# Kernel optimization log

Measured on AMD Instinct MI355X. Metric: run time of the kernel, lower is better.

Reference implementation:

```python
import jax, jax.numpy as jnp
import numpy as np

N, E = 100000, 1600000
F1, H1, H2 = 128, 128, 128


def setup_inputs() -> dict:
    key = jax.random.key(0)
    ks = jax.random.split(key, 8)
    x = jax.random.normal(ks[0], (N, F1), dtype=jnp.float32)
    edge_index = jax.random.randint(ks[1], (2, E), 0, N, dtype=jnp.int64)
    s1 = 1.0 / np.sqrt(F1)
    s2 = 1.0 / np.sqrt(H1)
    s3 = 1.0 / np.sqrt(H2)
    W1 = jax.random.uniform(ks[2], (F1, H1), jnp.float32, -s1, s1)
    b1 = jax.random.uniform(ks[3], (H1,), jnp.float32, -s1, s1)
    W2 = jax.random.uniform(ks[4], (H1, H2), jnp.float32, -s2, s2)
    b2 = jax.random.uniform(ks[5], (H2,), jnp.float32, -s2, s2)
    Wc = jax.random.uniform(ks[6], (H2, 1), jnp.float32, -s3, s3)
    bc = jax.random.uniform(ks[7], (1,), jnp.float32, -s3, s3)
    return {"x": x, "edge_index": edge_index, "W1": W1, "b1": b1,
            "W2": W2, "b2": b2, "Wc": Wc, "bc": bc}


def _gcn_conv(h, W, b, row, col, norm, n):
    # linear transform then degree-normalized gather/scatter-add aggregation
    h = h @ W                                  # [N, out]
    msg = h[row] * norm[:, None]               # [E+N, out] gather + scale
    out = jax.ops.segment_sum(msg, col, num_segments=n)  # scatter-add
    return out + b


def reference(x, edge_index, W1, b1, W2, b2, Wc, bc):
    n = x.shape[0]
    loops = jnp.arange(n, dtype=edge_index.dtype)
    row = jnp.concatenate([edge_index[0], loops])  # sources (with self-loops)
    col = jnp.concatenate([edge_index[1], loops])  # targets (with self-loops)
    deg = jax.ops.segment_sum(jnp.ones_like(col, dtype=x.dtype), col,
                              num_segments=n)
    dinv = jnp.where(deg > 0, jax.lax.rsqrt(deg), 0.0)
    norm = dinv[row] * dinv[col]                   # symmetric normalization

    h = jnp.tanh(_gcn_conv(x, W1, b1, row, col, norm, n))
    h = jnp.tanh(_gcn_conv(h, W2, b2, row, col, norm, n))
    logits = (h @ Wc + bc)[:, 0]                   # [N]
    return jax.nn.softmax(logits)                  # softmax over all nodes
```

## Files before the change

### kernel.cpp

```cpp
#include <hip/hip_runtime.h>
#include <hip/hip_fp16.h>


#define BSHIFT 9
#define BSPAN  512
#define PCHUNK 4096
#define LCAP   12288
#define BPAD   4096

typedef _Float16 half8 __attribute__((ext_vector_type(8)));
typedef float floatx4 __attribute__((ext_vector_type(4)));
typedef float floatx2 __attribute__((ext_vector_type(2)));

__device__ inline float tanh_fast(float x) {
    float e = __expf(2.0f * x);
    return 1.0f - 2.0f * __builtin_amdgcn_rcpf(e + 1.0f);
}

__device__ inline void fp8_acc8(floatx2* acc, uint2 v) {
    acc[0] += __builtin_amdgcn_cvt_pk_f32_fp8((int)v.x, false);
    acc[1] += __builtin_amdgcn_cvt_pk_f32_fp8((int)v.x, true);
    acc[2] += __builtin_amdgcn_cvt_pk_f32_fp8((int)v.y, false);
    acc[3] += __builtin_amdgcn_cvt_pk_f32_fp8((int)v.y, true);
}

__global__ __launch_bounds__(256) void hist_buckets(const int* __restrict__ col, int E,
                                                    int* __restrict__ bucketCnt) {
    __shared__ int h[256];
    h[threadIdx.x] = 0;
    __syncthreads();
    for (int e = blockIdx.x * 256 + threadIdx.x; e < E; e += gridDim.x * 256)
        atomicAdd(&h[col[e] >> BSHIFT], 1);
    __syncthreads();
    int v = h[threadIdx.x];
    if (v) atomicAdd(&bucketCnt[threadIdx.x], v);
}

__global__ void scan_buckets(const int* __restrict__ cnt, int* __restrict__ bucketPtr,
                             int* __restrict__ cursor, int NB, int E) {
    __shared__ int s[256];
    int t = threadIdx.x;
    int v = (t < NB) ? cnt[t] : 0;
    s[t] = v;
    __syncthreads();
    for (int d = 1; d < 256; d <<= 1) {
        int x = (t >= d) ? s[t - d] : 0;
        __syncthreads();
        s[t] += x;
        __syncthreads();
    }
    if (t < NB) {
        int p = s[t] - v;
        bucketPtr[t] = p;
        cursor[t] = p;
    }
    if (t == 0) bucketPtr[NB] = E;
}

__global__ __launch_bounds__(256) void partition_edges(const int* __restrict__ row,
                                                       const int* __restrict__ col, int E,
                                                       int* __restrict__ cursor,
                                                       unsigned int* __restrict__ pairs) {
    __shared__ int hist[256], sscan[256], gdelta[256], hcur[256];
    __shared__ uint2 stage[PCHUNK];
    int t = threadIdx.x;
    int base = blockIdx.x * PCHUNK;
    int cnt = min(PCHUNK, E - base);
    hist[t] = 0;
    __syncthreads();
    uint2 v[16];
    int b_[16];
#pragma unroll
    for (int k = 0; k < 16; k++) {
        int idx = t + k * 256;
        if (idx < cnt) {
            int c = col[base + idx], r = row[base + idx];
            v[k] = make_uint2((unsigned)c, (unsigned)r);
            b_[k] = c >> BSHIFT;
            atomicAdd(&hist[b_[k]], 1);
        } else b_[k] = -1;
    }
    __syncthreads();
    int hv = hist[t];
    sscan[t] = hv;
    __syncthreads();
    for (int d = 1; d < 256; d <<= 1) {
        int x = (t >= d) ? sscan[t - d] : 0;
        __syncthreads();
        sscan[t] += x;
        __syncthreads();
    }
    int excl = sscan[t] - hv;
    if (hv > 0) {
        int g = atomicAdd(&cursor[t], hv);
        gdelta[t] = g - excl;
    }
    hcur[t] = excl;
    __syncthreads();
#pragma unroll
    for (int k = 0; k < 16; k++) {
        if (b_[k] >= 0) {
            int slot = atomicAdd(&hcur[b_[k]], 1);
            stage[slot] = v[k];
        }
    }
    __syncthreads();
    for (int i = t; i < cnt; i += 256) {
        uint2 p = stage[i];
        pairs[gdelta[p.x >> BSHIFT] + i] = (p.y << BSHIFT) | (p.x & (BSPAN - 1));
    }
}

__global__ __launch_bounds__(256) void build_bucket_csr(const unsigned int* __restrict__ pairs,
                                                        const int* __restrict__ bucketPtr,
                                                        int* __restrict__ rowptrP,
                                                        int* __restrict__ rowEndP,
                                                        float* __restrict__ dinv,
                                                        int* __restrict__ csrP,
                                                        int n, int NB, int E) {
    __shared__ int hist[BSPAN];
    __shared__ int lptr[BSPAN];
    __shared__ int s[256];
    __shared__ int srcStage[LCAP];
    __shared__ int totp;
    int b = blockIdx.x, t = threadIdx.x;
    int base = bucketPtr[b], cnt = bucketPtr[b + 1] - base;
    int baseP = base + b * BPAD;
    int node0 = b << BSHIFT;
    int nn = min(BSPAN, n - node0);
    hist[t] = 0; hist[t + 256] = 0;
    __syncthreads();
    for (int i = t; i < cnt; i += 256)
        atomicAdd(&hist[pairs[base + i] & (BSPAN - 1)], 1);
    __syncthreads();
    int d0 = (2 * t < nn)     ? ((hist[2 * t] + 8) & ~7)     : 0;
    int d1 = (2 * t + 1 < nn) ? ((hist[2 * t + 1] + 8) & ~7) : 0;
    int sum = d0 + d1;
    s[t] = sum;
    __syncthreads();
    for (int d = 1; d < 256; d <<= 1) {
        int x = (t >= d) ? s[t - d] : 0;
        __syncthreads();
        s[t] += x;
        __syncthreads();
    }
    int excl = s[t] - sum;
    lptr[2 * t] = excl;
    lptr[2 * t + 1] = excl + d0;
    if (t == 255) totp = s[255];
    __syncthreads();
    int cntp = totp;
    for (int lc = t; lc < nn; lc += 256) {
        int st = baseP + lptr[lc];
        int dP = (hist[lc] + 8) & ~7;
        rowptrP[node0 + lc] = st;
        rowEndP[node0 + lc] = st + dP;
        dinv[node0 + lc] = rsqrtf((float)(hist[lc] + 1));
    }
    __syncthreads();
    bool inLds = (cntp <= LCAP);
    if (inLds) {
        for (int i = t; i < cntp; i += 256) srcStage[i] = n;
        __syncthreads();
        for (int lc = t; lc < nn; lc += 256) srcStage[lptr[lc]] = node0 + lc;
        hist[t] = 1; hist[t + 256] = 1;
        __syncthreads();
        for (int i = t; i < cnt; i += 256) {
            unsigned int p = pairs[base + i];
            int lc = p & (BSPAN - 1);
            int rank = atomicAdd(&hist[lc], 1);
            srcStage[lptr[lc] + rank] = (int)(p >> BSHIFT);
        }
        __syncthreads();
        for (int i = t; i < cntp; i += 256) csrP[baseP + i] = srcStage[i];
    } else {
        for (int i = t; i < cntp; i += 256) csrP[baseP + i] = n;
        __syncthreads();
        for (int lc = t; lc < nn; lc += 256) csrP[baseP + lptr[lc]] = node0 + lc;
        hist[t] = 1; hist[t + 256] = 1;
        __syncthreads();
        for (int i = t; i < cnt; i += 256) {
            unsigned int p = pairs[base + i];
            int lc = p & (BSPAN - 1);
            int rank = atomicAdd(&hist[lc], 1);
            csrP[baseP + lptr[lc] + rank] = (int)(p >> BSHIFT);
        }
    }
}

__global__ __launch_bounds__(256) void prep_wfrags(const float* __restrict__ W1,
                                                   const float* __restrict__ W2,
                                                   uint4* __restrict__ F1,
                                                   uint4* __restrict__ F2,
                                                   unsigned char* __restrict__ T1,
                                                   unsigned char* __restrict__ T2, int n) {
    int g = blockIdx.x * 256 + threadIdx.x;
    if (g >= 4096) {
        int t = g - 4096;
        uint4 z = make_uint4(0, 0, 0, 0);
        if (t < 8) ((uint4*)(T1 + (size_t)n * 128))[t] = z;
        else if (t < 16) ((uint4*)(T2 + (size_t)n * 128))[t - 8] = z;
        return;
    }
    bool second = (g >= 2048);
    const float* W = second ? W2 : W1;
    uint4* F = second ? F2 : F1;
    int t = g & 2047;
    int lane = t & 63, ct = (t >> 6) & 7, ks = t >> 9;
    int col = ct * 16 + (lane & 15);
    int kb = ks * 32 + (lane >> 4) * 8;
    half8 v;
#pragma unroll
    for (int j = 0; j < 8; j++) {
        int k = kb + j;
        int krow = second ? (((k & 7) << 4) | (k >> 3)) : k;
        v[j] = (_Float16)W[krow * 128 + col];
    }
    F[t] = __builtin_bit_cast(uint4, v);
}

template <bool HALF_IN>
__global__ __launch_bounds__(256) void gemm_mfma(const void* __restrict__ Ap,
                                                 const uint4* __restrict__ F,
                                                 const float* __restrict__ dinv,
                                                 unsigned char* __restrict__ T8, int n) {
    int w = threadIdx.x >> 6, lane = threadIdx.x & 63;
    int r0 = blockIdx.x * 128 + w * 32;
    int rA0 = r0 + (lane & 15);
    int rA1 = rA0 + 16;
    int kc = lane >> 4;
    floatx4 acc[2][8] = {};

#pragma unroll
    for (int ks = 0; ks < 4; ks++) {
        half8 a0 = {}, a1 = {};
        if constexpr (HALF_IN) {
            const uint4* A4 = (const uint4*)Ap;
            if (rA0 < n) a0 = __builtin_bit_cast(half8, A4[(size_t)rA0 * 16 + ks * 4 + kc]);
            if (rA1 < n) a1 = __builtin_bit_cast(half8, A4[(size_t)rA1 * 16 + ks * 4 + kc]);
        } else {
            const float* Af = (const float*)Ap;
            if (rA0 < n) {
                const float4* p = (const float4*)&Af[(size_t)rA0 * 128 + ks * 32 + kc * 8];
                float4 u = p[0], v = p[1];
                a0[0] = (_Float16)u.x; a0[1] = (_Float16)u.y; a0[2] = (_Float16)u.z; a0[3] = (_Float16)u.w;
                a0[4] = (_Float16)v.x; a0[5] = (_Float16)v.y; a0[6] = (_Float16)v.z; a0[7] = (_Float16)v.w;
            }
            if (rA1 < n) {
                const float4* p = (const float4*)&Af[(size_t)rA1 * 128 + ks * 32 + kc * 8];
                float4 u = p[0], v = p[1];
                a1[0] = (_Float16)u.x; a1[1] = (_Float16)u.y; a1[2] = (_Float16)u.z; a1[3] = (_Float16)u.w;
                a1[4] = (_Float16)v.x; a1[5] = (_Float16)v.y; a1[6] = (_Float16)v.z; a1[7] = (_Float16)v.w;
            }
        }
        half8 b[8];
#pragma unroll
        for (int ct = 0; ct < 8; ct++)
            b[ct] = __builtin_bit_cast(half8, F[ks * 512 + ct * 64 + lane]);
#pragma unroll
        for (int ct = 0; ct < 8; ct++) {
            acc[0][ct] = __builtin_amdgcn_mfma_f32_16x16x32_f16(a0, b[ct], acc[0][ct], 0, 0, 0);
            acc[1][ct] = __builtin_amdgcn_mfma_f32_16x16x32_f16(a1, b[ct], acc[1][ct], 0, 0, 0);
        }
    }

    int c = lane & 15;
#pragma unroll
    for (int rt = 0; rt < 2; rt++) {
        int rbase = r0 + rt * 16 + (lane >> 4) * 4;
#pragma unroll
        for (int reg = 0; reg < 4; reg++) {
            int r = rbase + reg;
            if (r < n) {
                float di = dinv[r];
                float vv[8];
#pragma unroll
                for (int ct = 0; ct < 8; ct++) vv[ct] = acc[rt][ct][reg] * di;
                int d0 = __builtin_amdgcn_cvt_pk_fp8_f32(vv[0], vv[1], 0, false);
                d0 = __builtin_amdgcn_cvt_pk_fp8_f32(vv[2], vv[3], d0, true);
                int d1 = __builtin_amdgcn_cvt_pk_fp8_f32(vv[4], vv[5], 0, false);
                d1 = __builtin_amdgcn_cvt_pk_fp8_f32(vv[6], vv[7], d1, true);
                *(uint2*)(T8 + (size_t)r * 128 + c * 8) = make_uint2((unsigned)d0, (unsigned)d1);
            }
        }
    }
}

__global__ __launch_bounds__(256) void aggregate(const unsigned char* __restrict__ T8,
                                                 const int* __restrict__ csrP,
                                                 const int* __restrict__ rowptrP,
                                                 const int* __restrict__ rowEndP,
                                                 const float* __restrict__ dinv,
                                                 const float* __restrict__ bias,
                                                 unsigned int* __restrict__ Out, int n) {
    int node = (int)((blockIdx.x * 256 + threadIdx.x) >> 6);
    int lane = threadIdx.x & 63;
    if (node >= n) return;
    int grp = lane >> 4, m = lane & 15;
    unsigned mo = (unsigned)m << 3;

    floatx2 acc[4] = {}, acc2[4] = {};
    int e = rowptrP[node], end = rowEndP[node];
    while (e < end) {
        int take = min(end - e, 64);
#pragma unroll 2
        for (int j = 0; j < take; j += 8) {
            int sA = csrP[e + j + grp];
            int sB = csrP[e + j + 4 + grp];
            uint2 vA = *(const uint2*)(T8 + (((unsigned)sA << 7) | mo));
            uint2 vB = *(const uint2*)(T8 + (((unsigned)sB << 7) | mo));
            fp8_acc8(acc, vA);
            fp8_acc8(acc2, vB);
        }
        e += take;
    }
#pragma unroll
    for (int q = 0; q < 4; q++) acc[q] += acc2[q];
    float* af = (float*)acc;
#pragma unroll
    for (int q = 0; q < 8; q++) {
        af[q] += __shfl_xor(af[q], 16);
        af[q] += __shfl_xor(af[q], 32);
    }

    floatx2 a = acc[grp];
    int dim = (grp << 5) | m;
    float di = dinv[node];
    float o0 = tanh_fast(a.x * di + bias[dim]);
    float o1 = tanh_fast(a.y * di + bias[dim + 16]);
    Out[(size_t)node * 64 + m * 4 + grp] =
        __builtin_bit_cast(unsigned int, __floats2half2_rn(o0, o1));
}

__global__ __launch_bounds__(256) void aggregate_logits(const unsigned char* __restrict__ T8,
                                                        const int* __restrict__ csrP,
                                                        const int* __restrict__ rowptrP,
                                                        const int* __restrict__ rowEndP,
                                                        const float* __restrict__ dinv,
                                                        const float* __restrict__ bias,
                                                        const float* __restrict__ Wc,
                                                        const float* __restrict__ bc,
                                                        float* __restrict__ logits, int n) {
    int node = (int)((blockIdx.x * 256 + threadIdx.x) >> 6);
    int lane = threadIdx.x & 63;
    if (node >= n) return;
    int grp = lane >> 4, m = lane & 15;
    unsigned mo = (unsigned)m << 3;

    floatx2 acc[4] = {}, acc2[4] = {};
    int e = rowptrP[node], end = rowEndP[node];
    while (e < end) {
        int take = min(end - e, 64);
#pragma unroll 2
        for (int j = 0; j < take; j += 8) {
            int sA = csrP[e + j + grp];
            int sB = csrP[e + j + 4 + grp];
            uint2 vA = *(const uint2*)(T8 + (((unsigned)sA << 7) | mo));
            uint2 vB = *(const uint2*)(T8 + (((unsigned)sB << 7) | mo));
            fp8_acc8(acc, vA);
            fp8_acc8(acc2, vB);
        }
        e += take;
    }
#pragma unroll
    for (int q = 0; q < 4; q++) acc[q] += acc2[q];
    float* af = (float*)acc;
#pragma unroll
    for (int q = 0; q < 8; q++) {
        af[q] += __shfl_xor(af[q], 16);
        af[q] += __shfl_xor(af[q], 32);
    }

    floatx2 a = acc[grp];
    int dim = (grp << 5) | m;
    float di = dinv[node];
    float d = tanh_fast(a.x * di + bias[dim]) * Wc[dim]
            + tanh_fast(a.y * di + bias[dim + 16]) * Wc[dim + 16];
#pragma unroll
    for (int off = 1; off < 64; off <<= 1) d += __shfl_xor(d, off);
    if (lane == 0) logits[node] = d + bc[0];
}

__global__ __launch_bounds__(256) void maxpart(const float* __restrict__ logits, int n,
                                               float* __restrict__ partialMax,
                                               float* __restrict__ denom) {
    if (blockIdx.x == 0 && threadIdx.x == 0) *denom = 0.0f;
    __shared__ float s[256];
    float m = -3.4e38f;
    for (int i = blockIdx.x * 256 + threadIdx.x; i < n; i += 256 * 256)
        m = fmaxf(m, logits[i]);
    s[threadIdx.x] = m;
    __syncthreads();
    for (int d = 128; d; d >>= 1) {
        if (threadIdx.x < d) s[threadIdx.x] = fmaxf(s[threadIdx.x], s[threadIdx.x + d]);
        __syncthreads();
    }
    if (threadIdx.x == 0) partialMax[blockIdx.x] = s[0];
}

__global__ __launch_bounds__(256) void exp_kernel(const float* __restrict__ logits,
                                                  const float* __restrict__ partialMax,
                                                  float* __restrict__ outv,
                                                  float* __restrict__ denom, int n) {
    __shared__ float s[256];
    s[threadIdx.x] = partialMax[threadIdx.x];
    __syncthreads();
    for (int d = 128; d; d >>= 1) {
        if (threadIdx.x < d) s[threadIdx.x] = fmaxf(s[threadIdx.x], s[threadIdx.x + d]);
        __syncthreads();
    }
    float maxv = s[0];
    __syncthreads();
    int i = blockIdx.x * 256 + threadIdx.x;
    float e = 0.0f;
    if (i < n) {
        e = expf(logits[i] - maxv);
        outv[i] = e;
    }
    s[threadIdx.x] = e;
    __syncthreads();
    for (int d = 128; d; d >>= 1) {
        if (threadIdx.x < d) s[threadIdx.x] += s[threadIdx.x + d];
        __syncthreads();
    }
    if (threadIdx.x == 0) atomicAdd(denom, s[0]);
}

__global__ __launch_bounds__(256) void norm_kernel(float* __restrict__ out,
                                                   const float* __restrict__ denom, int n) {
    int i = blockIdx.x * 256 + threadIdx.x;
    if (i < n) out[i] = out[i] / (*denom);
}

extern "C" void kernel_launch(void* const* d_in, const int* in_sizes, int n_in,
                              void* d_out, int out_size, void* d_ws, size_t ws_size,
                              hipStream_t stream) {
    const float* x  = (const float*)d_in[0];
    const int*   ei = (const int*)d_in[1];
    const float* W1 = (const float*)d_in[2];
    const float* b1 = (const float*)d_in[3];
    const float* W2 = (const float*)d_in[4];
    const float* b2 = (const float*)d_in[5];
    const float* Wc = (const float*)d_in[6];
    const float* bc = (const float*)d_in[7];

    int n = in_sizes[0] / 128;
    int E = in_sizes[1] / 2;
    const int* row = ei;
    const int* col = ei + E;
    int NB = (n + BSPAN - 1) >> BSHIFT;

    char* ws = (char*)d_ws;
    size_t off = 0;
    auto alloc = [&](size_t bytes) -> void* {
        void* p = ws + off;
        off += (bytes + 255) & ~(size_t)255;
        return p;
    };
    unsigned char* T1 = (unsigned char*)alloc((size_t)(n + 1) * 128);
    unsigned char* T2 = (unsigned char*)alloc((size_t)(n + 1) * 128);
    unsigned int*  H1 = (unsigned int*)alloc((size_t)n * 128 * 2);
    int*    csrP     = (int*)alloc(((size_t)E + (size_t)NB * BPAD + 64) * 4);
    unsigned int* pairs = (unsigned int*)alloc((size_t)E * 4);
    float*  dinv     = (float*)alloc((size_t)n * 4);
    int*    rowptrP  = (int*)alloc((size_t)(n + 1) * 4);
    int*    rowEndP  = (int*)alloc((size_t)n * 4);
    int*    bucketCnt= (int*)alloc(256 * 4);
    int*    bucketPtr= (int*)alloc(257 * 4);
    int*    cursor   = (int*)alloc(256 * 4);
    uint4*  F1       = (uint4*)alloc(2048 * 16);
    uint4*  F2       = (uint4*)alloc(2048 * 16);
    float*  logits   = (float*)alloc((size_t)n * 4);
    float*  pmax     = (float*)alloc(256 * 4);
    float*  denom    = (float*)alloc(4);

    int nbN = (n + 255) / 256;
    int nbW = (n + 3) / 4;
    int nbG = (n + 127) / 128;

    hipMemsetAsync(bucketCnt, 0, 256 * 4, stream);

    hist_buckets<<<512, 256, 0, stream>>>(col, E, bucketCnt);
    scan_buckets<<<1, 256, 0, stream>>>(bucketCnt, bucketPtr, cursor, NB, E);
    partition_edges<<<(E + PCHUNK - 1) / PCHUNK, 256, 0, stream>>>(row, col, E, cursor, pairs);
    prep_wfrags<<<17, 256, 0, stream>>>(W1, W2, F1, F2, T1, T2, n);
    build_bucket_csr<<<NB, 256, 0, stream>>>(pairs, bucketPtr, rowptrP, rowEndP, dinv,
                                             csrP, n, NB, E);

    gemm_mfma<false><<<nbG, 256, 0, stream>>>(x, F1, dinv, T1, n);
    aggregate<<<nbW, 256, 0, stream>>>(T1, csrP, rowptrP, rowEndP, dinv, b1, H1, n);
    gemm_mfma<true><<<nbG, 256, 0, stream>>>(H1, F2, dinv, T2, n);
    aggregate_logits<<<nbW, 256, 0, stream>>>(T2, csrP, rowptrP, rowEndP, dinv, b2, Wc, bc,
                                              logits, n);

    maxpart<<<256, 256, 0, stream>>>(logits, n, pmax, denom);
    exp_kernel<<<nbN, 256, 0, stream>>>(logits, pmax, (float*)d_out, denom, n);
    norm_kernel<<<nbN, 256, 0, stream>>>((float*)d_out, denom, n);
}
```

Measured before the change: 200.7 us.

## Map two nodes per wavefront in aggregation and shrink CSR padding to 4

The aggregation kernels now give each node half a wavefront (32 lanes) instead of a full 64-lane wave. Each half processes 4 edges per step rather than 8. CSR row padding drops from multiples of 8 to multiples of 4, and the per-bucket pad shrinks to match. This cuts wasted loads of padding edges on low-degree nodes, which are common at average degree about 16, and reduces the cross-lane reduction work. In exchange, each lane issues fewer memory loads in flight per iteration, and the inner loop is no longer unrolled.

```diff
diff --git a/kernel.cpp b/kernel.cpp
--- a/kernel.cpp
+++ b/kernel.cpp
@@ -6,7 +6,7 @@
 #define BSPAN  512
 #define PCHUNK 4096
 #define LCAP   12288
-#define BPAD   4096
+#define BPAD   2048
 
 typedef _Float16 half8 __attribute__((ext_vector_type(8)));
 typedef float floatx4 __attribute__((ext_vector_type(4)));
@@ -133,8 +133,8 @@
     for (int i = t; i < cnt; i += 256)
         atomicAdd(&hist[pairs[base + i] & (BSPAN - 1)], 1);
     __syncthreads();
-    int d0 = (2 * t < nn)     ? ((hist[2 * t] + 8) & ~7)     : 0;
-    int d1 = (2 * t + 1 < nn) ? ((hist[2 * t + 1] + 8) & ~7) : 0;
+    int d0 = (2 * t < nn)     ? ((hist[2 * t] + 4) & ~3)     : 0;
+    int d1 = (2 * t + 1 < nn) ? ((hist[2 * t + 1] + 4) & ~3) : 0;
     int sum = d0 + d1;
     s[t] = sum;
     __syncthreads();
@@ -152,7 +152,7 @@
     int cntp = totp;
     for (int lc = t; lc < nn; lc += 256) {
         int st = baseP + lptr[lc];
-        int dP = (hist[lc] + 8) & ~7;
+        int dP = (hist[lc] + 4) & ~3;
         rowptrP[node0 + lc] = st;
         rowEndP[node0 + lc] = st + dP;
         dinv[node0 + lc] = rsqrtf((float)(hist[lc] + 1));
@@ -293,43 +293,44 @@
                                                  const float* __restrict__ dinv,
                                                  const float* __restrict__ bias,
                                                  unsigned int* __restrict__ Out, int n) {
-    int node = (int)((blockIdx.x * 256 + threadIdx.x) >> 6);
     int lane = threadIdx.x & 63;
-    if (node >= n) return;
-    int grp = lane >> 4, m = lane & 15;
+    int half = lane >> 5;
+    int node = (int)((blockIdx.x * 256 + threadIdx.x) >> 6) * 2 + half;
+    int grp2 = (lane >> 4) & 1, m = lane & 15;
     unsigned mo = (unsigned)m << 3;
 
     floatx2 acc[4] = {}, acc2[4] = {};
-    int e = rowptrP[node], end = rowEndP[node];
+    int e = 0, end = 0;
+    if (node < n) { e = rowptrP[node]; end = rowEndP[node]; }
     while (e < end) {
-        int take = min(end - e, 64);
-#pragma unroll 2
-        for (int j = 0; j < take; j += 8) {
-            int sA = csrP[e + j + grp];
-            int sB = csrP[e + j + 4 + grp];
-            uint2 vA = *(const uint2*)(T8 + (((unsigned)sA << 7) | mo));
-            uint2 vB = *(const uint2*)(T8 + (((unsigned)sB << 7) | mo));
-            fp8_acc8(acc, vA);
-            fp8_acc8(acc2, vB);
-        }
-        e += take;
+        int sA = csrP[e + grp2];
+        int sB = csrP[e + 2 + grp2];
+        uint2 vA = *(const uint2*)(T8 + (((unsigned)sA << 7) | mo));
+        uint2 vB = *(const uint2*)(T8 + (((unsigned)sB << 7) | mo));
+        fp8_acc8(acc, vA);
+        fp8_acc8(acc2, vB);
+        e += 4;
     }
 #pragma unroll
     for (int q = 0; q < 4; q++) acc[q] += acc2[q];
     float* af = (float*)acc;
 #pragma unroll
-    for (int q = 0; q < 8; q++) {
-        af[q] += __shfl_xor(af[q], 16);
-        af[q] += __shfl_xor(af[q], 32);
-    }
-
-    floatx2 a = acc[grp];
-    int dim = (grp << 5) | m;
-    float di = dinv[node];
-    float o0 = tanh_fast(a.x * di + bias[dim]);
-    float o1 = tanh_fast(a.y * di + bias[dim + 16]);
-    Out[(size_t)node * 64 + m * 4 + grp] =
-        __builtin_bit_cast(unsigned int, __floats2half2_rn(o0, o1));
+    for (int q = 0; q < 8; q++) af[q] += __shfl_xor(af[q], 16);
+
+    if (node < n) {
+        float di = dinv[node];
+        floatx2 aL = acc[grp2], aH = acc[grp2 + 2];
+        int dimL = (grp2 << 5) | m;
+        int dimH = ((grp2 + 2) << 5) | m;
+        float o0 = tanh_fast(aL.x * di + bias[dimL]);
+        float o1 = tanh_fast(aL.y * di + bias[dimL + 16]);
+        float o2 = tanh_fast(aH.x * di + bias[dimH]);
+        float o3 = tanh_fast(aH.y * di + bias[dimH + 16]);
+        Out[(size_t)node * 64 + m * 4 + grp2] =
+            __builtin_bit_cast(unsigned int, __floats2half2_rn(o0, o1));
+        Out[(size_t)node * 64 + m * 4 + grp2 + 2] =
+            __builtin_bit_cast(unsigned int, __floats2half2_rn(o2, o3));
+    }
 }
 
 __global__ __launch_bounds__(256) void aggregate_logits(const unsigned char* __restrict__ T8,
@@ -341,44 +342,44 @@
                                                         const float* __restrict__ Wc,
                                                         const float* __restrict__ bc,
                                                         float* __restrict__ logits, int n) {
-    int node = (int)((blockIdx.x * 256 + threadIdx.x) >> 6);
     int lane = threadIdx.x & 63;
-    if (node >= n) return;
-    int grp = lane >> 4, m = lane & 15;
+    int half = lane >> 5;
+    int node = (int)((blockIdx.x * 256 + threadIdx.x) >> 6) * 2 + half;
+    int grp2 = (lane >> 4) & 1, m = lane & 15;
     unsigned mo = (unsigned)m << 3;
 
     floatx2 acc[4] = {}, acc2[4] = {};
-    int e = rowptrP[node], end = rowEndP[node];
+    int e = 0, end = 0;
+    if (node < n) { e = rowptrP[node]; end = rowEndP[node]; }
     while (e < end) {
-        int take = min(end - e, 64);
-#pragma unroll 2
-        for (int j = 0; j < take; j += 8) {
-            int sA = csrP[e + j + grp];
-            int sB = csrP[e + j + 4 + grp];
-            uint2 vA = *(const uint2*)(T8 + (((unsigned)sA << 7) | mo));
-            uint2 vB = *(const uint2*)(T8 + (((unsigned)sB << 7) | mo));
-            fp8_acc8(acc, vA);
-            fp8_acc8(acc2, vB);
-        }
-        e += take;
+        int sA = csrP[e + grp2];
+        int sB = csrP[e + 2 + grp2];
+        uint2 vA = *(const uint2*)(T8 + (((unsigned)sA << 7) | mo));
+        uint2 vB = *(const uint2*)(T8 + (((unsigned)sB << 7) | mo));
+        fp8_acc8(acc, vA);
+        fp8_acc8(acc2, vB);
+        e += 4;
     }
 #pragma unroll
     for (int q = 0; q < 4; q++) acc[q] += acc2[q];
     float* af = (float*)acc;
 #pragma unroll
-    for (int q = 0; q < 8; q++) {
-        af[q] += __shfl_xor(af[q], 16);
-        af[q] += __shfl_xor(af[q], 32);
-    }
-
-    floatx2 a = acc[grp];
-    int dim = (grp << 5) | m;
-    float di = dinv[node];
-    float d = tanh_fast(a.x * di + bias[dim]) * Wc[dim]
-            + tanh_fast(a.y * di + bias[dim + 16]) * Wc[dim + 16];
-#pragma unroll
-    for (int off = 1; off < 64; off <<= 1) d += __shfl_xor(d, off);
-    if (lane == 0) logits[node] = d + bc[0];
+    for (int q = 0; q < 8; q++) af[q] += __shfl_xor(af[q], 16);
+
+    float d = 0.0f;
+    if (node < n) {
+        float di = dinv[node];
+        floatx2 aL = acc[grp2], aH = acc[grp2 + 2];
+        int dimL = (grp2 << 5) | m;
+        int dimH = ((grp2 + 2) << 5) | m;
+        d = tanh_fast(aL.x * di + bias[dimL]) * Wc[dimL]
+          + tanh_fast(aL.y * di + bias[dimL + 16]) * Wc[dimL + 16]
+          + tanh_fast(aH.x * di + bias[dimH]) * Wc[dimH]
+          + tanh_fast(aH.y * di + bias[dimH + 16]) * Wc[dimH + 16];
+    }
+#pragma unroll
+    for (int off = 1; off < 32; off <<= 1) d += __shfl_xor(d, off);
+    if ((lane & 31) == 0 && node < n) logits[node] = d + bc[0];
 }
 
 __global__ __launch_bounds__(256) void maxpart(const float* __restrict__ logits, int n,
@@ -475,7 +476,7 @@
     float*  denom    = (float*)alloc(4);
 
     int nbN = (n + 255) / 256;
-    int nbW = (n + 3) / 4;
+    int nbW = (n + 7) / 8;
     int nbG = (n + 127) / 128;
 
     hipMemsetAsync(bucketCnt, 0, 256 * 4, stream);
```

Result: no change. 201.6 us (+0.5%).
